# Performance work log

Hardware: AMD Instinct MI355X
Metric: run time of the kernel (lower is better)

## Reference

```python
import jax, jax.numpy as jnp
import numpy as np

N_HEAD = 12
N_EMBD = 768


def setup_inputs() -> dict:
    key = jax.random.key(0)
    ks = jax.random.split(key, 5)
    B, T, C = 8, 1024, N_EMBD
    x = jax.random.normal(ks[0], (B, T, C), dtype=jnp.float32)
    # c_attn: Linear(C, 3C); c_proj: Linear(C, C). PyTorch Linear: y = x @ W.T + b
    s = 1.0 / np.sqrt(C)
    W_attn = jax.random.uniform(ks[1], (3 * C, C), minval=-s, maxval=s, dtype=jnp.float32)
    b_attn = jax.random.uniform(ks[2], (3 * C,), minval=-s, maxval=s, dtype=jnp.float32)
    W_proj = jax.random.uniform(ks[3], (C, C), minval=-s, maxval=s, dtype=jnp.float32)
    b_proj = jax.random.uniform(ks[4], (C,), minval=-s, maxval=s, dtype=jnp.float32)
    return {"x": x, "W_attn": W_attn, "b_attn": b_attn, "W_proj": W_proj, "b_proj": b_proj}


def reference(x, W_attn, b_attn, W_proj, b_proj):
    B, T, C = x.shape
    H = N_HEAD
    hs = C // H  # head size
    qkv = x @ W_attn.T + b_attn  # [B, T, 3C]
    q, k, v = jnp.split(qkv, 3, axis=2)
    # [B, T, H, hs] -> [B, H, T, hs]
    q = q.reshape(B, T, H, hs).transpose(0, 2, 1, 3)
    k = k.reshape(B, T, H, hs).transpose(0, 2, 1, 3)
    v = v.reshape(B, T, H, hs).transpose(0, 2, 1, 3)
    att = jnp.einsum('bhqd,bhkd->bhqk', q, k) * (1.0 / np.sqrt(hs))
    causal = jnp.tril(jnp.ones((T, T), dtype=bool))
    att = jnp.where(causal, att, -jnp.inf)
    att = jax.nn.softmax(att, axis=-1)
    y = jnp.einsum('bhqk,bhkd->bhqd', att, v)  # [B, H, T, hs]
    y = y.transpose(0, 2, 1, 3).reshape(B, T, C)
    return y @ W_proj.T + b_proj
```

## Files before the change

### kernel.cpp

```cpp
#include <hip/hip_runtime.h>

typedef unsigned short u16;
typedef unsigned int u32;
typedef unsigned long long u64;
typedef __attribute__((ext_vector_type(8))) __bf16 bf16x8;
typedef __attribute__((ext_vector_type(4))) float f32x4;
typedef __attribute__((ext_vector_type(4))) int i32x4;

#define MFMA16(a, b, c) __builtin_amdgcn_mfma_f32_16x16x32_bf16(a, b, c, 0, 0, 0)

__device__ __forceinline__ u16 f2b(float f) {
  __bf16 h = (__bf16)f;
  return __builtin_bit_cast(u16, h);
}

__device__ __forceinline__ float mx3(float a, float b, float c) {
  return fmaxf(fmaxf(a, b), c);
}

__device__ __forceinline__ void gl_lds16(const void* g, void* l) {
  __builtin_amdgcn_global_load_lds(
      (const __attribute__((address_space(1))) void*)g,
      (__attribute__((address_space(3))) void*)l, 16, 0, 0);
}

__device__ __forceinline__ bf16x8 ldf(const void* p) {
  return __builtin_bit_cast(bf16x8, *(const i32x4*)p);
}

__global__ __launch_bounds__(256) void cvt3_kernel(
    const float4* __restrict__ a, ushort4* __restrict__ oa, int na4,
    const float4* __restrict__ b, ushort4* __restrict__ ob, int nb4,
    const float4* __restrict__ c, ushort4* __restrict__ oc, int nc4) {
  const int step = gridDim.x * blockDim.x;
  const int t0 = blockIdx.x * blockDim.x + threadIdx.x;
  for (int i = t0; i < na4; i += step) {
    float4 v = a[i];
    ushort4 o; o.x = f2b(v.x); o.y = f2b(v.y); o.z = f2b(v.z); o.w = f2b(v.w);
    oa[i] = o;
  }
  for (int i = t0; i < nb4; i += step) {
    float4 v = b[i];
    ushort4 o; o.x = f2b(v.x); o.y = f2b(v.y); o.z = f2b(v.z); o.w = f2b(v.w);
    ob[i] = o;
  }
  for (int i = t0; i < nc4; i += step) {
    float4 v = c[i];
    ushort4 o; o.x = f2b(v.x); o.y = f2b(v.y); o.z = f2b(v.z); o.w = f2b(v.w);
    oc[i] = o;
  }
}

template <int BM, int EPI>
__global__ __launch_bounds__(256, 3) void gemm4(
    const u16* __restrict__ A, const u16* __restrict__ B,
    const float* __restrict__ bias, int M, int N, int K,
    u16* __restrict__ q_s, u16* __restrict__ k_s, u16* __restrict__ vt_s,
    float* __restrict__ outf) {
  constexpr int BN = 192;
  constexpr int MR = BM / 32;
  constexpr int NR = 6;
  constexpr int IA = BM / 32;
  constexpr int IB = 6;
  __shared__ __align__(16) u16 As[BM * 64];
  __shared__ __align__(16) u16 Bs[BN * 64];
  const int tid = threadIdx.x;
  const int w = tid >> 6, l = tid & 63;
  const int lo = l & 15, hi = l >> 4;
  const int wr = w >> 1, wc = w & 1;
  const int nwg = gridDim.x * gridDim.y;
  int bid = blockIdx.y * gridDim.x + blockIdx.x;
  bid = (bid & 7) * (nwg >> 3) + (bid >> 3);
  const int bm0 = (bid / gridDim.x) * BM;
  const int bn0 = (bid % gridDim.x) * BN;
  const size_t Kb = (size_t)K * 2;
  const char* Ab = (const char*)A;
  const char* Bb = (const char*)B;
  const int lrow8 = l >> 3;
  const int lcol = (l & 7) * 16;

  f32x4 acc[MR][NR] = {};

  for (int kt = 0; kt < K; kt += 64) {
    __syncthreads();
#pragma unroll
    for (int i = 0; i < IA; ++i) {
      int rl = (w * IA + i) * 8 + lrow8;
      int cb = lcol ^ ((rl & 7) << 4);
      gl_lds16(Ab + (size_t)(bm0 + rl) * Kb + kt * 2 + cb,
               (char*)As + (w * IA + i) * 1024);
    }
#pragma unroll
    for (int i = 0; i < IB; ++i) {
      int rl = (w * IB + i) * 8 + lrow8;
      int cb = lcol ^ ((rl & 7) << 4);
      gl_lds16(Bb + (size_t)(bn0 + rl) * Kb + kt * 2 + cb,
               (char*)Bs + (w * IB + i) * 1024);
    }
    __syncthreads();
#pragma unroll
    for (int ks = 0; ks < 2; ++ks) {
      bf16x8 bfr[NR];
#pragma unroll
      for (int nf = 0; nf < NR; ++nf) {
        int r = wc * 96 + nf * 16 + lo;
        bfr[nf] = ldf((char*)Bs + r * 128 + ((ks * 64 + hi * 16) ^ ((r & 7) << 4)));
      }
#pragma unroll
      for (int mf = 0; mf < MR; ++mf) {
        int r = wr * (MR * 16) + mf * 16 + lo;
        bf16x8 afr = ldf((char*)As + r * 128 + ((ks * 64 + hi * 16) ^ ((r & 7) << 4)));
#pragma unroll
        for (int nf = 0; nf < NR; ++nf) acc[mf][nf] = MFMA16(afr, bfr[nf], acc[mf][nf]);
      }
    }
  }

#pragma unroll
  for (int nf = 0; nf < NR; ++nf) {
    int col = bn0 + wc * 96 + nf * 16 + lo;
    float bv = bias[col];
    if (EPI == 0) {
      int seg = col / 768;
      int cs = col - seg * 768;
      int h = cs >> 6, d = cs & 63;
      u16* dst = (seg == 0) ? q_s : k_s;
#pragma unroll
      for (int mf = 0; mf < MR; ++mf) {
        int m0 = bm0 + wr * (MR * 16) + mf * 16 + hi * 4;
        int bb = m0 >> 10, t0 = m0 & 1023;
        size_t bh = (size_t)(bb * 12 + h);
        if (seg < 2) {
#pragma unroll
          for (int r = 0; r < 4; ++r)
            dst[(bh * 1024 + t0 + r) * 64 + d] = f2b(acc[mf][nf][r] + bv);
        } else {
          ushort4 pk;
          pk.x = f2b(acc[mf][nf][0] + bv);
          pk.y = f2b(acc[mf][nf][1] + bv);
          pk.z = f2b(acc[mf][nf][2] + bv);
          pk.w = f2b(acc[mf][nf][3] + bv);
          *(ushort4*)&vt_s[(bh * 64 + d) * 1024 + t0] = pk;
        }
      }
    } else {
#pragma unroll
      for (int mf = 0; mf < MR; ++mf) {
        int m0 = bm0 + wr * (MR * 16) + mf * 16 + hi * 4;
#pragma unroll
        for (int r = 0; r < 4; ++r) outf[(size_t)(m0 + r) * N + col] = acc[mf][nf][r] + bv;
      }
    }
  }
}

__global__ __launch_bounds__(256) void attn_kernel(
    const u16* __restrict__ Q, const u16* __restrict__ Kg,
    const u16* __restrict__ Vt, u16* __restrict__ Y) {
  __shared__ __align__(16) u16 Ks[2][64 * 64];
  __shared__ __align__(16) u16 Vs[2][64 * 64];
  __shared__ __align__(16) u16 Ps[4][16 * 64];
  const int tid = threadIdx.x;
  const int w = tid >> 6, l = tid & 63;
  const int lo = l & 15, hi = l >> 4;
  int bid = blockIdx.y * gridDim.x + blockIdx.x;
  bid = (bid & 7) * 96 + (bid >> 3);
  const int bh = bid >> 3;
  const int pr = bid & 7;
  const int b = bh / 12, h = bh % 12;
  const float c1 = 0.125f * 1.44269504f;
  char* pw = (char*)&Ps[w][0];
  const int swl = (lo & 7) << 4;
  const u16* Qb = Q + (size_t)bh * 65536;
  const char* Kbp = (const char*)(Kg + (size_t)bh * 65536);
  const char* Vbp = (const char*)(Vt + (size_t)bh * 65536);

  bf16x8 onesv;
#pragma unroll
  for (int j = 0; j < 8; ++j) onesv[j] = (__bf16)1.0f;

  auto STAGE = [&](int buf, int kb) {
#pragma unroll
    for (int i = 0; i < 2; ++i) {
      int c = w * 2 + i;
      int row = c * 8 + (l >> 3);
      int cb = ((l & 7) * 16) ^ ((row & 7) << 4);
      gl_lds16(Kbp + (size_t)(kb + row) * 128 + cb, (char*)&Ks[buf][0] + c * 1024);
      gl_lds16(Vbp + (size_t)row * 2048 + (size_t)kb * 2 + cb, (char*)&Vs[buf][0] + c * 1024);
    }
  };

  for (int sg = 0; sg < 2; ++sg) {
    const int tile = sg ? (15 - pr) : pr;
    const int q0 = tile * 64 + w * 16;
    const int nt = tile + 1;
    const int qr = q0 + lo;

    bf16x8 qf[2];
#pragma unroll
    for (int ks = 0; ks < 2; ++ks)
      qf[ks] = ldf(Qb + (size_t)(q0 + lo) * 64 + ks * 32 + hi * 8);

    f32x4 o[4] = {};
    f32x4 lsum = {0.f, 0.f, 0.f, 0.f};
    float mrow = -1e30f;

    __builtin_amdgcn_s_barrier();
    STAGE(0, 0);
    for (int kt = 0; kt < nt; ++kt) {
      const int cur = kt & 1;
      asm volatile("s_waitcnt vmcnt(0)" ::: "memory");
      __builtin_amdgcn_s_barrier();
      __builtin_amdgcn_sched_barrier(0);
      if (kt + 1 < nt) STAGE(cur ^ 1, (kt + 1) * 64);
      const char* Kt = (const char*)&Ks[cur][0];
      const char* Vv = (const char*)&Vs[cur][0];
      const int kb = kt * 64;

      f32x4 st[4] = {};
      __builtin_amdgcn_s_setprio(1);
#pragma unroll
      for (int kf = 0; kf < 4; ++kf) {
        int rb = (kf * 16 + lo) * 128;
#pragma unroll
        for (int ks = 0; ks < 2; ++ks)
          st[kf] = MFMA16(ldf(Kt + rb + ((ks * 64 + hi * 16) ^ swl)), qf[ks], st[kf]);
      }
      __builtin_amdgcn_s_setprio(0);
      bf16x8 vb[4][2];
#pragma unroll
      for (int nd = 0; nd < 4; ++nd) {
        int rb = (nd * 16 + lo) * 128;
#pragma unroll
        for (int ks = 0; ks < 2; ++ks)
          vb[nd][ks] = ldf(Vv + rb + ((ks * 64 + hi * 16) ^ swl));
      }
      if (kt == nt - 1) {
#pragma unroll
        for (int kf = 0; kf < 4; ++kf)
#pragma unroll
          for (int r = 0; r < 4; ++r) {
            int kcol = kb + kf * 16 + hi * 4 + r;
            if (kcol > qr) st[kf][r] = -1e30f;
          }
      }
      float t0 = mx3(st[0][0], st[0][1], st[0][2]);
      float t1 = mx3(st[0][3], st[1][0], st[1][1]);
      float t2 = mx3(st[1][2], st[1][3], st[2][0]);
      float t3 = mx3(st[2][1], st[2][2], st[2][3]);
      float t4 = mx3(st[3][0], st[3][1], st[3][2]);
      float lm = fmaxf(mx3(t0, t1, t2), mx3(t3, t4, st[3][3]));
      if (__any(lm * c1 > mrow + 8.0f)) {
        float LM = fmaxf(lm, __shfl_xor(lm, 16));
        LM = fmaxf(LM, __shfl_xor(LM, 32));
        float Mn = fmaxf(mrow, LM * c1);
        float alP = __builtin_amdgcn_exp2f(mrow - Mn);
        mrow = Mn;
        f32x4 alo;
#pragma unroll
        for (int r = 0; r < 4; ++r) alo[r] = __shfl(alP, hi * 4 + r);
#pragma unroll
        for (int nd = 0; nd < 4; ++nd)
#pragma unroll
          for (int r = 0; r < 4; ++r) o[nd][r] *= alo[r];
#pragma unroll
        for (int r = 0; r < 4; ++r) lsum[r] *= alo[r];
      }
#pragma unroll
      for (int kf = 0; kf < 4; ++kf)
#pragma unroll
        for (int r = 0; r < 4; ++r)
          st[kf][r] = __builtin_amdgcn_exp2f(fmaf(st[kf][r], c1, -mrow));
#pragma unroll
      for (int kf = 0; kf < 4; ++kf) {
        u32 w0 = (u32)f2b(st[kf][0]) | ((u32)f2b(st[kf][1]) << 16);
        u32 w1 = (u32)f2b(st[kf][2]) | ((u32)f2b(st[kf][3]) << 16);
        *(u64*)(pw + lo * 128 + ((kf * 32 + hi * 8) ^ swl)) =
            (u64)w0 | ((u64)w1 << 32);
      }
      bf16x8 pa[2];
#pragma unroll
      for (int ks = 0; ks < 2; ++ks)
        pa[ks] = ldf(pw + lo * 128 + ((ks * 64 + hi * 16) ^ swl));
      __builtin_amdgcn_s_setprio(1);
#pragma unroll
      for (int ks = 0; ks < 2; ++ks) {
#pragma unroll
        for (int nd = 0; nd < 4; ++nd) o[nd] = MFMA16(pa[ks], vb[nd][ks], o[nd]);
        lsum = MFMA16(pa[ks], onesv, lsum);
      }
      __builtin_amdgcn_s_setprio(0);
      __builtin_amdgcn_sched_barrier(0);
    }

    f32x4 inv;
#pragma unroll
    for (int r = 0; r < 4; ++r) inv[r] = 1.0f / lsum[r];
#pragma unroll
    for (int nd = 0; nd < 4; ++nd)
#pragma unroll
      for (int r = 0; r < 4; ++r) {
        int t = q0 + hi * 4 + r;
        int d = nd * 16 + lo;
        Y[((size_t)b * 1024 + t) * 768 + h * 64 + d] = f2b(o[nd][r] * inv[r]);
      }
  }
}

extern "C" void kernel_launch(void* const* d_in, const int* in_sizes, int n_in,
                              void* d_out, int out_size, void* d_ws, size_t ws_size,
                              hipStream_t stream) {
  const float* x  = (const float*)d_in[0];
  const float* Wa = (const float*)d_in[1];
  const float* ba = (const float*)d_in[2];
  const float* Wp = (const float*)d_in[3];
  const float* bp = (const float*)d_in[4];
  float* out = (float*)d_out;
  char* ws = (char*)d_ws;

  constexpr size_t XB  = 0;
  constexpr size_t WAB = 12582912;
  constexpr size_t WPB = WAB + 3538944;
  constexpr size_t QS  = WPB + 1179648;
  constexpr size_t KS  = QS + 12582912;
  constexpr size_t VTS = KS + 12582912;
  constexpr size_t YB  = VTS + 12582912;

  u16* xb  = (u16*)(ws + XB);
  u16* wab = (u16*)(ws + WAB);
  u16* wpb = (u16*)(ws + WPB);
  u16* qs  = (u16*)(ws + QS);
  u16* ks  = (u16*)(ws + KS);
  u16* vts = (u16*)(ws + VTS);
  u16* yb  = (u16*)(ws + YB);

  cvt3_kernel<<<2048, 256, 0, stream>>>(
      (const float4*)x,  (ushort4*)xb,  8192 * 768 / 4,
      (const float4*)Wa, (ushort4*)wab, 2304 * 768 / 4,
      (const float4*)Wp, (ushort4*)wpb, 768 * 768 / 4);

  gemm4<128, 0><<<dim3(12, 64), 256, 0, stream>>>(xb, wab, ba, 8192, 2304, 768,
                                                  qs, ks, vts, nullptr);
  attn_kernel<<<dim3(8, 96), 256, 0, stream>>>(qs, ks, vts, yb);
  gemm4<64, 1><<<dim3(4, 128), 256, 0, stream>>>(yb, wpb, bp, 8192, 768, 768,
                                                 nullptr, nullptr, nullptr, out);
}
```

Before: 96.35 us.

## Fuse fp32-to-bf16 conversion of x into the QKV GEMM A-tile load

Drops the separate pass that converts x to bf16 and instead loads fp32 x directly in the QKV GEMM, converting to bf16 in registers before writing swizzled tiles to LDS. This removes one write and one read of a 12MB bf16 copy and shrinks the conversion kernel to weights only. In exchange the GEMM reads twice the bytes for A across its 12 column blocks, and it uses synchronous register loads plus LDS stores rather than async global_load_lds.

```diff
diff --git a/kernel.cpp b/kernel.cpp
--- a/kernel.cpp
+++ b/kernel.cpp
@@ -28,10 +28,9 @@
   return __builtin_bit_cast(bf16x8, *(const i32x4*)p);
 }
 
-__global__ __launch_bounds__(256) void cvt3_kernel(
+__global__ __launch_bounds__(256) void cvt2_kernel(
     const float4* __restrict__ a, ushort4* __restrict__ oa, int na4,
-    const float4* __restrict__ b, ushort4* __restrict__ ob, int nb4,
-    const float4* __restrict__ c, ushort4* __restrict__ oc, int nc4) {
+    const float4* __restrict__ b, ushort4* __restrict__ ob, int nb4) {
   const int step = gridDim.x * blockDim.x;
   const int t0 = blockIdx.x * blockDim.x + threadIdx.x;
   for (int i = t0; i < na4; i += step) {
@@ -44,16 +43,11 @@
     ushort4 o; o.x = f2b(v.x); o.y = f2b(v.y); o.z = f2b(v.z); o.w = f2b(v.w);
     ob[i] = o;
   }
-  for (int i = t0; i < nc4; i += step) {
-    float4 v = c[i];
-    ushort4 o; o.x = f2b(v.x); o.y = f2b(v.y); o.z = f2b(v.z); o.w = f2b(v.w);
-    oc[i] = o;
-  }
-}
-
-template <int BM, int EPI>
+}
+
+template <int BM, int EPI, int AF32>
 __global__ __launch_bounds__(256, 3) void gemm4(
-    const u16* __restrict__ A, const u16* __restrict__ B,
+    const void* __restrict__ Av, const u16* __restrict__ B,
     const float* __restrict__ bias, int M, int N, int K,
     u16* __restrict__ q_s, u16* __restrict__ k_s, u16* __restrict__ vt_s,
     float* __restrict__ outf) {
@@ -74,7 +68,6 @@
   const int bm0 = (bid / gridDim.x) * BM;
   const int bn0 = (bid % gridDim.x) * BN;
   const size_t Kb = (size_t)K * 2;
-  const char* Ab = (const char*)A;
   const char* Bb = (const char*)B;
   const int lrow8 = l >> 3;
   const int lcol = (l & 7) * 16;
@@ -83,12 +76,31 @@
 
   for (int kt = 0; kt < K; kt += 64) {
     __syncthreads();
-#pragma unroll
-    for (int i = 0; i < IA; ++i) {
-      int rl = (w * IA + i) * 8 + lrow8;
-      int cb = lcol ^ ((rl & 7) << 4);
-      gl_lds16(Ab + (size_t)(bm0 + rl) * Kb + kt * 2 + cb,
-               (char*)As + (w * IA + i) * 1024);
+    if constexpr (AF32) {
+      const float* Af = (const float*)Av;
+#pragma unroll
+      for (int i = 0; i < IA; ++i) {
+        int rl = (w * IA + i) * 8 + lrow8;
+        const float4* src =
+            (const float4*)(Af + (size_t)(bm0 + rl) * K + kt + (l & 7) * 8);
+        float4 a0 = src[0], a1 = src[1];
+        u32 q0 = (u32)f2b(a0.x) | ((u32)f2b(a0.y) << 16);
+        u32 q1 = (u32)f2b(a0.z) | ((u32)f2b(a0.w) << 16);
+        u32 q2 = (u32)f2b(a1.x) | ((u32)f2b(a1.y) << 16);
+        u32 q3 = (u32)f2b(a1.z) | ((u32)f2b(a1.w) << 16);
+        i32x4 pk = {(int)q0, (int)q1, (int)q2, (int)q3};
+        *(i32x4*)((char*)As + (w * IA + i) * 1024 + lrow8 * 128 +
+                  (lcol ^ (lrow8 << 4))) = pk;
+      }
+    } else {
+      const char* Ab = (const char*)Av;
+#pragma unroll
+      for (int i = 0; i < IA; ++i) {
+        int rl = (w * IA + i) * 8 + lrow8;
+        int cb = lcol ^ ((rl & 7) << 4);
+        gl_lds16(Ab + (size_t)(bm0 + rl) * Kb + kt * 2 + cb,
+                 (char*)As + (w * IA + i) * 1024);
+      }
     }
 #pragma unroll
     for (int i = 0; i < IB; ++i) {
@@ -318,15 +330,13 @@
   float* out = (float*)d_out;
   char* ws = (char*)d_ws;
 
-  constexpr size_t XB  = 0;
-  constexpr size_t WAB = 12582912;
+  constexpr size_t WAB = 0;
   constexpr size_t WPB = WAB + 3538944;
   constexpr size_t QS  = WPB + 1179648;
   constexpr size_t KS  = QS + 12582912;
   constexpr size_t VTS = KS + 12582912;
   constexpr size_t YB  = VTS + 12582912;
 
-  u16* xb  = (u16*)(ws + XB);
   u16* wab = (u16*)(ws + WAB);
   u16* wpb = (u16*)(ws + WPB);
   u16* qs  = (u16*)(ws + QS);
@@ -334,14 +344,13 @@
   u16* vts = (u16*)(ws + VTS);
   u16* yb  = (u16*)(ws + YB);
 
-  cvt3_kernel<<<2048, 256, 0, stream>>>(
-      (const float4*)x,  (ushort4*)xb,  8192 * 768 / 4,
+  cvt2_kernel<<<1024, 256, 0, stream>>>(
       (const float4*)Wa, (ushort4*)wab, 2304 * 768 / 4,
       (const float4*)Wp, (ushort4*)wpb, 768 * 768 / 4);
 
-  gemm4<128, 0><<<dim3(12, 64), 256, 0, stream>>>(xb, wab, ba, 8192, 2304, 768,
-                                                  qs, ks, vts, nullptr);
+  gemm4<128, 0, 1><<<dim3(12, 64), 256, 0, stream>>>(
+      (const void*)x, wab, ba, 8192, 2304, 768, qs, ks, vts, nullptr);
   attn_kernel<<<dim3(8, 96), 256, 0, stream>>>(qs, ks, vts, yb);
-  gemm4<64, 1><<<dim3(4, 128), 256, 0, stream>>>(yb, wpb, bp, 8192, 768, 768,
-                                                 nullptr, nullptr, nullptr, out);
-}
+  gemm4<64, 1, 0><<<dim3(4, 128), 256, 0, stream>>>(
+      (const void*)yb, wpb, bp, 8192, 768, 768, nullptr, nullptr, nullptr, out);
+}
```

New measurement: 99.62 us. 3.4% more time.
